# Performance work log

Measured on AMD Instinct MI355X. Metric: run time of the kernel, lower is better.

The kernel has to match this reference:

```python
import jax, jax.numpy as jnp
import numpy as np

B, D, S, H, L = 256, 7, 32, 512, 128  # batch, tree depth, n_symbols, hidden_size, latent_size
N = 2 ** D - 1  # nodes in complete binary tree, heap order (children of i are 2i+1, 2i+2)


def _xavier(key, shape):
    lim = float(np.sqrt(6.0 / (shape[0] + shape[1])))
    return jax.random.uniform(key, shape, jnp.float32, -lim, lim)


def setup_inputs():
    key = jax.random.key(0)
    ks = jax.random.split(key, 18)
    return {
        'symbols': jax.random.randint(ks[0], (B, N), 0, S, dtype=jnp.int32),
        'eps': jax.random.normal(ks[1], (B, L), jnp.float32),
        # Encoder GRU221: gate order [r, z, n], input weights act on one-hot symbol, hidden weights on cat(h_l, h_r)
        'ewi': _xavier(ks[2], (3 * H, S)),
        'ebi': jax.random.uniform(ks[3], (3 * H,), jnp.float32, -0.05, 0.05),
        'ewh': _xavier(ks[4], (3 * H, 2 * H)),
        'ebh': jax.random.uniform(ks[5], (3 * H,), jnp.float32, -0.05, 0.05),
        'h2mu_w': _xavier(ks[6], (L, H)),
        'h2mu_b': jax.random.uniform(ks[7], (L,), jnp.float32, -0.05, 0.05),
        'h2lv_w': _xavier(ks[8], (L, H)),
        'h2lv_b': jax.random.uniform(ks[9], (L,), jnp.float32, -0.05, 0.05),
        # Decoder
        'z2h_w': _xavier(ks[10], (H, L)),
        'z2h_b': jax.random.uniform(ks[11], (H,), jnp.float32, -0.05, 0.05),
        'h2o_w': _xavier(ks[12], (S, H)),
        'h2o_b': jax.random.uniform(ks[13], (S,), jnp.float32, -0.05, 0.05),
        # Decoder GRU122: gate order [r, z, n], each gate has 2H outputs (left/right child)
        'dwi': _xavier(ks[14], (6 * H, S)),
        'dbi': jax.random.uniform(ks[15], (6 * H,), jnp.float32, -0.05, 0.05),
        'dwh': _xavier(ks[16], (6 * H, H)),
        'dbh': jax.random.uniform(ks[17], (6 * H,), jnp.float32, -0.05, 0.05),
    }


def _hvae_forward(symbols, eps, ewi, ebi, ewh, ebh, h2mu_w, h2mu_b, h2lv_w, h2lv_b,
                  z2h_w, z2h_b, h2o_w, h2o_b, dwi, dbi, dwh, dbh):
    x_all = jax.nn.one_hot(symbols, S, dtype=jnp.float32)  # [B, N, S] node targets

    # ---- Encoder: GRU221 applied bottom-up, one batched step per tree level ----
    h = jnp.zeros((B, 2 ** D, H), jnp.float32)  # (absent) children of the deepest level
    for d in range(D - 1, -1, -1):
        n_d = 2 ** d
        x = x_all[:, n_d - 1: 2 * n_d - 1]       # [B, n_d, S] level-d symbols (heap order)
        hl, hr = h[:, 0::2], h[:, 1::2]           # [B, n_d, H] left/right child hiddens
        hcat = jnp.concatenate([hl, hr], axis=-1)
        gi = x @ ewi.T + ebi                       # [B, n_d, 3H]
        gh = hcat @ ewh.T + ebh
        r = jax.nn.sigmoid(gi[..., :H] + gh[..., :H])
        zg = jax.nn.sigmoid(gi[..., H:2 * H] + gh[..., H:2 * H])
        n = jnp.tanh(gi[..., 2 * H:] + r * gh[..., 2 * H:])
        h = (1.0 - zg) * n + zg * (hl + hr) * 0.5
    root = h[:, 0]                                 # [B, H]
    mu = root @ h2mu_w.T + h2mu_b                  # [B, L]
    logvar = root @ h2lv_w.T + h2lv_b
    zlat = mu + eps * jnp.exp(0.5 * logvar)        # reparameterized sample

    # ---- Decoder: GRU122 applied top-down, one batched step per tree level ----
    hidden = (zlat @ z2h_w.T + z2h_b)[:, None, :]  # [B, 1, H] root hidden
    preds = []
    for d in range(D):
        pred = hidden @ h2o_w.T + h2o_b            # [B, 2^d, S]
        preds.append(pred)
        if d < D - 1:
            a = jax.nn.softmax(pred, axis=-1)
            gi = a @ dwi.T + dbi                    # [B, 2^d, 6H]
            gh = hidden @ dwh.T + dbh
            r = jax.nn.sigmoid(gi[..., :2 * H] + gh[..., :2 * H])
            zg = jax.nn.sigmoid(gi[..., 2 * H:4 * H] + gh[..., 2 * H:4 * H])
            n = jnp.tanh(gi[..., 4 * H:] + r * gh[..., 4 * H:])
            dh = jnp.concatenate([hidden, hidden], axis=-1)  # h.repeat(1,1,2)
            out = (1.0 - zg) * n + zg * dh          # [B, 2^d, 2H]
            # torch.split -> (left, right); interleave as next level's hiddens (heap order)
            hidden = jnp.stack([out[..., :H], out[..., H:]], axis=2).reshape(B, 2 ** (d + 1), H)
    preds = jnp.concatenate(preds, axis=1)          # [B, N, S] per-node logits, level order
    return mu, logvar, preds


def reference(symbols, eps, ewi, ebi, ewh, ebh, h2mu_w, h2mu_b, h2lv_w, h2lv_b,
              z2h_w, z2h_b, h2o_w, h2o_b, dwi, dbi, dwh, dbh):
    return _hvae_forward(symbols, eps, ewi, ebi, ewh, ebh, h2mu_w, h2mu_b, h2lv_w, h2lv_b,
                         z2h_w, z2h_b, h2o_w, h2o_b, dwi, dbi, dwh, dbh)
```

## Files before the change

kernel.cpp:

```cpp
#include <hip/hip_runtime.h>
#include <hip/hip_bf16.h>

typedef unsigned short u16;
typedef unsigned int u32;
typedef __attribute__((ext_vector_type(8))) short short8;
typedef __attribute__((ext_vector_type(4))) float f32x4;

#define WAITV(N) asm volatile("s_waitcnt vmcnt(" #N ")" ::: "memory")

__device__ __forceinline__ float sigmoidf_(float x) { return 1.0f / (1.0f + expf(-x)); }
__device__ __forceinline__ float fsig(float x) {
    return __builtin_amdgcn_rcpf(1.0f + __expf(-x));
}
__device__ __forceinline__ float ftanh(float x) {
    x = fminf(fmaxf(x, -15.0f), 15.0f);
    float t = __expf(2.0f * x);
    return (t - 1.0f) * __builtin_amdgcn_rcpf(t + 1.0f);
}

__device__ __forceinline__ float bf2f(u16 u) {
    union { u32 i; float f; } v; v.i = ((u32)u) << 16; return v.f;
}
__device__ __forceinline__ u16 f2bf(float f) {
    union { float f; u32 i; } v; v.f = f;
    u32 lsb = (v.i >> 16) & 1u;
    v.i += 0x7fffu + lsb;
    return (u16)(v.i >> 16);
}

__device__ __forceinline__ void gload16(const u16* g, u16* l) {
    __builtin_amdgcn_global_load_lds(
        (const __attribute__((address_space(1))) u32*)g,
        (__attribute__((address_space(3))) u32*)l, 16, 0, 0);
}

__global__ __launch_bounds__(256) void prep(
    const float* __restrict__ ewh, const float* __restrict__ dwh,
    const float* __restrict__ dwi, const float* __restrict__ ewi,
    const float* __restrict__ h2o_w, const int* __restrict__ symbols,
    const float* __restrict__ ebi, const float* __restrict__ ebh,
    u16* __restrict__ ewh_b, u16* __restrict__ dwh_b, u16* __restrict__ dwi_b,
    u16* __restrict__ ewi_b, u16* __restrict__ wo_b, u16* __restrict__ oneh,
    u16* __restrict__ ltab)
{
    int idx = blockIdx.x * 256 + threadIdx.x;
    if (idx < 1572864) { ewh_b[idx] = f2bf(ewh[idx]); return; }
    idx -= 1572864;
    if (idx < 1572864) { dwh_b[idx] = f2bf(dwh[idx]); return; }
    idx -= 1572864;
    if (idx < 98304) { dwi_b[idx] = f2bf(dwi[idx]); return; }
    idx -= 98304;
    if (idx < 49152) { ewi_b[idx] = f2bf(ewi[idx]); return; }
    idx -= 49152;
    if (idx < 16384) { wo_b[idx] = f2bf(h2o_w[idx]); return; }
    idx -= 16384;
    if (idx < 1040384) {
        int col = idx & 31, row = idx >> 5;
        oneh[idx] = (col == symbols[row]) ? (u16)0x3F80 : (u16)0;
        return;
    }
    idx -= 1040384;
    if (idx < 16384) {
        int c = idx & 511, sym = idx >> 9;
        float r = sigmoidf_(ewi[c * 32 + sym]          + ebi[c]        + ebh[c]);
        float z = sigmoidf_(ewi[(512 + c) * 32 + sym]  + ebi[512 + c]  + ebh[512 + c]);
        float n = tanhf(    ewi[(1024 + c) * 32 + sym] + ebi[1024 + c] + r * ebh[1024 + c]);
        ltab[idx] = f2bf((1.0f - z) * n);
    }
}

template<int RF, bool LEAF>
__global__ __launch_bounds__(256, 2) void enc_tile(
    const u16* __restrict__ A, const u16* __restrict__ W,
    const u16* __restrict__ oneh, const u16* __restrict__ Wi,
    const u16* __restrict__ tab, const int* __restrict__ symbols,
    const float* __restrict__ ebi, const float* __restrict__ ebh,
    u16* __restrict__ hout, int dlog, int node_base)
{
    constexpr int BM = RF * 32;
    constexpr int NCA = BM / 64;
    constexpr int NS = 32;
    __shared__ alignas(16) u16 Als[2][BM * 32];
    __shared__ alignas(16) u16 Bls[2][192 * 32];
    const int tid  = threadIdx.x;
    const int lane = tid & 63;
    const int wid  = tid >> 6;
    const int wr = wid >> 1, wc = wid & 1;
    const int lr = lane & 15, lk = lane >> 4;
    const int m0 = blockIdx.x * BM;
    const int c0 = blockIdx.y * 64;
    const int mask = (1 << dlog) - 1;

    size_t a_goff[NCA]; int a_loff[NCA];
    int symL[NCA], symR[NCA];
#pragma unroll
    for (int j = 0; j < NCA; ++j) {
        int a = wid * NCA + j;
        int r_ = a * 16 + (lane >> 2);
        int kps = (lane & 3) ^ ((r_ >> 1) & 3);
        a_loff[j] = a * 512 + lane * 8;
        if constexpr (LEAF) {
            int rg = m0 + r_;
            int b_ = rg >> dlog, jj = rg & mask;
            int cbase = b_ * 127 + 2 * (node_base + jj) + 1;
            symL[j] = symbols[cbase];
            symR[j] = symbols[cbase + 1];
            a_goff[j] = kps * 8;
        } else {
            a_goff[j] = (size_t)(m0 + r_) * 1024 + kps * 8;
            symL[j] = symR[j] = 0;
        }
    }
    size_t b_goff[3]; int b_loff[3];
#pragma unroll
    for (int j = 0; j < 3; ++j) {
        int b = wid * 3 + j;
        int rr = b * 16 + (lane >> 2);
        int kps = (lane & 3) ^ ((rr >> 1) & 3);
        int grow = (rr >> 6) * 512 + c0 + (rr & 63);
        b_goff[j] = (size_t)grow * 1024 + kps * 8;
        b_loff[j] = b * 512 + lane * 8;
    }
    int a_roff[RF];
#pragma unroll
    for (int i = 0; i < RF; ++i) {
        int row = wr * (RF * 16) + i * 16 + lr;
        a_roff[i] = row * 32 + (lk ^ ((row >> 1) & 3)) * 8;
    }
    int b_roff[3][2];
#pragma unroll
    for (int s = 0; s < 3; ++s)
#pragma unroll
        for (int cf = 0; cf < 2; ++cf) {
            int row = s * 64 + wc * 32 + cf * 16 + lr;
            b_roff[s][cf] = row * 32 + (lk ^ ((row >> 1) & 3)) * 8;
        }

    f32x4 acc[4][2][RF];
#pragma unroll
    for (int s = 0; s < 4; ++s)
#pragma unroll
        for (int cf = 0; cf < 2; ++cf)
#pragma unroll
            for (int i = 0; i < RF; ++i) acc[s][cf][i] = (f32x4){0.f, 0.f, 0.f, 0.f};

    auto issue = [&](int stg) {
        const int buf = stg & 1;
        const int nk = stg * 32;
#pragma unroll
        for (int j = 0; j < NCA; ++j) {
            if constexpr (LEAF) {
                const u16* src = (nk < 512)
                    ? tab + (size_t)symL[j] * 512 + nk + a_goff[j]
                    : tab + (size_t)symR[j] * 512 + (nk - 512) + a_goff[j];
                gload16(src, &Als[buf][a_loff[j]]);
            } else {
                gload16(A + a_goff[j] + nk, &Als[buf][a_loff[j]]);
            }
        }
#pragma unroll
        for (int j = 0; j < 3; ++j) gload16(W + b_goff[j] + nk, &Bls[buf][b_loff[j]]);
    };
    auto compute = [&](int buf) {
        short8 a[RF];
#pragma unroll
        for (int i = 0; i < RF; ++i)
            a[i] = *reinterpret_cast<const short8*>(&Als[buf][a_roff[i]]);
#pragma unroll
        for (int s = 0; s < 3; ++s)
#pragma unroll
            for (int cf = 0; cf < 2; ++cf) {
                short8 b = *reinterpret_cast<const short8*>(&Bls[buf][b_roff[s][cf]]);
#pragma unroll
                for (int i = 0; i < RF; ++i)
                    acc[s][cf][i] = __builtin_amdgcn_mfma_f32_16x16x32_bf16(b, a[i], acc[s][cf][i], 0, 0, 0);
            }
    };

    issue(0);
    WAITV(0);
    __builtin_amdgcn_s_barrier();
    for (int t = 0; t < NS - 1; ++t) {
        issue(t + 1);
        compute(t & 1);
        WAITV(0);
        __builtin_amdgcn_s_barrier();
    }
    compute((NS - 1) & 1);

    {
        short8 oh[RF];
#pragma unroll
        for (int i = 0; i < RF; ++i) {
            int m = m0 + wr * (RF * 16) + i * 16 + lr;
            int b_ = m >> dlog, j_ = m & mask;
            oh[i] = *reinterpret_cast<const short8*>(
                oneh + (size_t)(b_ * 127 + node_base + j_) * 32 + lk * 8);
        }
#pragma unroll
        for (int s = 0; s < 3; ++s) {
            const int d = (s == 2) ? 3 : s;
#pragma unroll
            for (int cf = 0; cf < 2; ++cf) {
                short8 wb = *reinterpret_cast<const short8*>(
                    Wi + (size_t)(s * 512 + c0 + wc * 32 + cf * 16 + lr) * 32 + lk * 8);
#pragma unroll
                for (int i = 0; i < RF; ++i)
                    acc[d][cf][i] = __builtin_amdgcn_mfma_f32_16x16x32_bf16(wb, oh[i], acc[d][cf][i], 0, 0, 0);
            }
        }
    }

    float4 ebr4[2], ebz4[2], ebin4[2], ebhn4[2];
    int cb[2];
#pragma unroll
    for (int cf = 0; cf < 2; ++cf) {
        cb[cf] = c0 + wc * 32 + cf * 16 + lk * 4;
        float4 bi0 = *reinterpret_cast<const float4*>(ebi + cb[cf]);
        float4 bh0 = *reinterpret_cast<const float4*>(ebh + cb[cf]);
        float4 bi1 = *reinterpret_cast<const float4*>(ebi + 512 + cb[cf]);
        float4 bh1 = *reinterpret_cast<const float4*>(ebh + 512 + cb[cf]);
        ebr4[cf] = make_float4(bi0.x + bh0.x, bi0.y + bh0.y, bi0.z + bh0.z, bi0.w + bh0.w);
        ebz4[cf] = make_float4(bi1.x + bh1.x, bi1.y + bh1.y, bi1.z + bh1.z, bi1.w + bh1.w);
        ebin4[cf] = *reinterpret_cast<const float4*>(ebi + 1024 + cb[cf]);
        ebhn4[cf] = *reinterpret_cast<const float4*>(ebh + 1024 + cb[cf]);
    }
#pragma unroll
    for (int i = 0; i < RF; ++i) {
        int m = m0 + wr * (RF * 16) + i * 16 + lr;
        int symLm = 0, symRm = 0;
        if constexpr (LEAF) {
            int b_ = m >> dlog, jj = m & mask;
            int cbase_ = b_ * 127 + 2 * (node_base + jj) + 1;
            symLm = symbols[cbase_];
            symRm = symbols[cbase_ + 1];
        }
#pragma unroll
        for (int cf = 0; cf < 2; ++cf) {
            ushort4 hl4, hr4;
            if constexpr (LEAF) {
                hl4 = *reinterpret_cast<const ushort4*>(tab + (size_t)symLm * 512 + cb[cf]);
                hr4 = *reinterpret_cast<const ushort4*>(tab + (size_t)symRm * 512 + cb[cf]);
            } else {
                hl4 = *reinterpret_cast<const ushort4*>(A + (size_t)m * 1024 + cb[cf]);
                hr4 = *reinterpret_cast<const ushort4*>(A + (size_t)m * 1024 + 512 + cb[cf]);
            }
            const float eb_r[4] = {ebr4[cf].x, ebr4[cf].y, ebr4[cf].z, ebr4[cf].w};
            const float eb_z[4] = {ebz4[cf].x, ebz4[cf].y, ebz4[cf].z, ebz4[cf].w};
            const float eb_in[4] = {ebin4[cf].x, ebin4[cf].y, ebin4[cf].z, ebin4[cf].w};
            const float eb_hn[4] = {ebhn4[cf].x, ebhn4[cf].y, ebhn4[cf].z, ebhn4[cf].w};
            const u16 hlv[4] = {hl4.x, hl4.y, hl4.z, hl4.w};
            const u16 hrv[4] = {hr4.x, hr4.y, hr4.z, hr4.w};
            ushort4 outv;
            u16* ov = reinterpret_cast<u16*>(&outv);
#pragma unroll
            for (int r = 0; r < 4; ++r) {
                float rr_ = fsig(acc[0][cf][i][r] + eb_r[r]);
                float zz  = fsig(acc[1][cf][i][r] + eb_z[r]);
                float nn  = ftanh(acc[3][cf][i][r] + eb_in[r] + rr_ * (acc[2][cf][i][r] + eb_hn[r]));
                float hm = (bf2f(hlv[r]) + bf2f(hrv[r])) * 0.5f;
                ov[r] = f2bf((1.0f - zz) * nn + zz * hm);
            }
            *reinterpret_cast<ushort4*>(hout + (size_t)m * 512 + cb[cf]) = outv;
        }
    }
}

__global__ __launch_bounds__(256) void mid1(
    const u16* __restrict__ root, const float* __restrict__ h2mu_w,
    const float* __restrict__ h2mu_b, const float* __restrict__ h2lv_w,
    const float* __restrict__ h2lv_b, const float* __restrict__ eps,
    float* __restrict__ zlat, float* __restrict__ out_mu,
    float* __restrict__ out_lv)
{
    int b = blockIdx.x, t = threadIdx.x;
    __shared__ float rs[512];
    rs[t]       = bf2f(root[(size_t)b * 512 + t]);
    rs[t + 256] = bf2f(root[(size_t)b * 512 + t + 256]);
    __syncthreads();
    const float* w = (t < 128) ? (h2mu_w + (size_t)t * 512) : (h2lv_w + (size_t)(t - 128) * 512);
    float acc = 0.0f;
    for (int k = 0; k < 512; ++k) acc += rs[k] * w[k];
    acc += (t < 128) ? h2mu_b[t] : h2lv_b[t - 128];
    __shared__ float vals[256];
    vals[t] = acc;
    __syncthreads();
    if (t < 128) {
        float mu = vals[t], lv = vals[t + 128];
        float zl = mu + eps[b * 128 + t] * expf(0.5f * lv);
        zlat[b * 128 + t] = zl;
        out_mu[b * 128 + t] = mu;
        out_lv[b * 128 + t] = lv;
    }
}

__global__ __launch_bounds__(512) void mid2(
    const float* __restrict__ zlat, const float* __restrict__ z2h_w,
    const float* __restrict__ z2h_b, u16* __restrict__ hidden)
{
    int b = blockIdx.x, t = threadIdx.x;
    __shared__ float zs[128];
    if (t < 128) zs[t] = zlat[b * 128 + t];
    __syncthreads();
    float acc = z2h_b[t];
    for (int k = 0; k < 128; ++k) acc += zs[k] * z2h_w[(size_t)t * 128 + k];
    hidden[(size_t)b * 512 + t] = f2bf(acc);
}

__global__ __launch_bounds__(256) void pred_mfma(
    const u16* __restrict__ hidden, const u16* __restrict__ Wo,
    const float* __restrict__ h2o_b, u16* __restrict__ aout,
    float* __restrict__ preds_out, int dlog, int node_base, int write_a)
{
    const int lane = threadIdx.x & 63;
    const int wid  = threadIdx.x >> 6;
    const int lr = lane & 15, lk = lane >> 4;
    const int m0 = blockIdx.x * 64 + wid * 16;

    f32x4 acc0 = (f32x4){0.f, 0.f, 0.f, 0.f};
    f32x4 acc1 = (f32x4){0.f, 0.f, 0.f, 0.f};
    const u16* Arow = hidden + (size_t)(m0 + lr) * 512 + lk * 8;
    const u16* B0 = Wo + (size_t)lr * 512 + lk * 8;
    const u16* B1 = Wo + (size_t)(16 + lr) * 512 + lk * 8;
#pragma unroll
    for (int k0 = 0; k0 < 512; k0 += 32) {
        short8 a  = *reinterpret_cast<const short8*>(Arow + k0);
        short8 b0 = *reinterpret_cast<const short8*>(B0 + k0);
        short8 b1 = *reinterpret_cast<const short8*>(B1 + k0);
        acc0 = __builtin_amdgcn_mfma_f32_16x16x32_bf16(b0, a, acc0, 0, 0, 0);
        acc1 = __builtin_amdgcn_mfma_f32_16x16x32_bf16(b1, a, acc1, 0, 0, 0);
    }
    float4 bb0 = *reinterpret_cast<const float4*>(h2o_b + lk * 4);
    float4 bb1 = *reinterpret_cast<const float4*>(h2o_b + 16 + lk * 4);
    float p0[4], p1[4];
    p0[0] = acc0[0] + bb0.x; p0[1] = acc0[1] + bb0.y; p0[2] = acc0[2] + bb0.z; p0[3] = acc0[3] + bb0.w;
    p1[0] = acc1[0] + bb1.x; p1[1] = acc1[1] + bb1.y; p1[2] = acc1[2] + bb1.z; p1[3] = acc1[3] + bb1.w;
    float mx = fmaxf(fmaxf(fmaxf(p0[0], p0[1]), fmaxf(p0[2], p0[3])),
                     fmaxf(fmaxf(p1[0], p1[1]), fmaxf(p1[2], p1[3])));
    mx = fmaxf(mx, __shfl_xor(mx, 16));
    mx = fmaxf(mx, __shfl_xor(mx, 32));
    float e0[4], e1[4], s = 0.0f;
#pragma unroll
    for (int r = 0; r < 4; ++r) { e0[r] = __expf(p0[r] - mx); e1[r] = __expf(p1[r] - mx); s += e0[r] + e1[r]; }
    s += __shfl_xor(s, 16);
    s += __shfl_xor(s, 32);

    int m = m0 + lr;
    int b_ = m >> dlog, j_ = m & ((1 << dlog) - 1);
    size_t o = (size_t)(b_ * 127 + node_base + j_) * 32;
    *reinterpret_cast<float4*>(preds_out + o + lk * 4)      = make_float4(p0[0], p0[1], p0[2], p0[3]);
    *reinterpret_cast<float4*>(preds_out + o + 16 + lk * 4) = make_float4(p1[0], p1[1], p1[2], p1[3]);
    if (write_a) {
        float inv = __builtin_amdgcn_rcpf(s);
        ushort4 a0, a1;
        u16* av0 = reinterpret_cast<u16*>(&a0);
        u16* av1 = reinterpret_cast<u16*>(&a1);
#pragma unroll
        for (int r = 0; r < 4; ++r) { av0[r] = f2bf(e0[r] * inv); av1[r] = f2bf(e1[r] * inv); }
        *reinterpret_cast<ushort4*>(aout + (size_t)m * 32 + lk * 4)      = a0;
        *reinterpret_cast<ushort4*>(aout + (size_t)m * 32 + 16 + lk * 4) = a1;
    }
}

template<int RF>
__global__ __launch_bounds__(256, 2) void dec_tile(
    const u16* __restrict__ Hin, const u16* __restrict__ aB,
    const u16* __restrict__ Wh, const u16* __restrict__ Wi,
    const float* __restrict__ dbh, const float* __restrict__ dbi,
    u16* __restrict__ Hout)
{
    constexpr int BM = RF * 32;
    constexpr int NCA = BM / 64;
    constexpr int NS = 16;
    __shared__ alignas(16) u16 Als[2][BM * 32];
    __shared__ alignas(16) u16 Bls[2][192 * 32];
    const int tid  = threadIdx.x;
    const int lane = tid & 63;
    const int wid  = tid >> 6;
    const int wr = wid >> 1, wc = wid & 1;
    const int lr = lane & 15, lk = lane >> 4;
    const int m0 = blockIdx.x * BM;
    const int c0 = blockIdx.y * 64;

    size_t a_goff[NCA]; int a_loff[NCA];
#pragma unroll
    for (int j = 0; j < NCA; ++j) {
        int a = wid * NCA + j;
        int r_ = a * 16 + (lane >> 2);
        int kps = (lane & 3) ^ ((r_ >> 1) & 3);
        a_goff[j] = (size_t)(m0 + r_) * 512 + kps * 8;
        a_loff[j] = a * 512 + lane * 8;
    }
    size_t b_goff[3]; int b_loff[3];
#pragma unroll
    for (int j = 0; j < 3; ++j) {
        int b = wid * 3 + j;
        int rr = b * 16 + (lane >> 2);
        int kps = (lane & 3) ^ ((rr >> 1) & 3);
        int grow = (rr >> 6) * 1024 + c0 + (rr & 63);
        b_goff[j] = (size_t)grow * 512 + kps * 8;
        b_loff[j] = b * 512 + lane * 8;
    }
    int a_roff[RF];
#pragma unroll
    for (int i = 0; i < RF; ++i) {
        int row = wr * (RF * 16) + i * 16 + lr;
        a_roff[i] = row * 32 + (lk ^ ((row >> 1) & 3)) * 8;
    }
    int b_roff[3][2];
#pragma unroll
    for (int s = 0; s < 3; ++s)
#pragma unroll
        for (int cf = 0; cf < 2; ++cf) {
            int row = s * 64 + wc * 32 + cf * 16 + lr;
            b_roff[s][cf] = row * 32 + (lk ^ ((row >> 1) & 3)) * 8;
        }

    f32x4 acc[4][2][RF];
#pragma unroll
    for (int s = 0; s < 4; ++s)
#pragma unroll
        for (int cf = 0; cf < 2; ++cf)
#pragma unroll
            for (int i = 0; i < RF; ++i) acc[s][cf][i] = (f32x4){0.f, 0.f, 0.f, 0.f};

    auto issue = [&](int stg) {
        const int buf = stg & 1;
        const int nk = stg * 32;
#pragma unroll
        for (int j = 0; j < NCA; ++j) gload16(Hin + a_goff[j] + nk, &Als[buf][a_loff[j]]);
#pragma unroll
        for (int j = 0; j < 3; ++j) gload16(Wh + b_goff[j] + nk, &Bls[buf][b_loff[j]]);
    };
    auto compute = [&](int buf) {
        short8 a[RF];
#pragma unroll
        for (int i = 0; i < RF; ++i)
            a[i] = *reinterpret_cast<const short8*>(&Als[buf][a_roff[i]]);
#pragma unroll
        for (int s = 0; s < 3; ++s)
#pragma unroll
            for (int cf = 0; cf < 2; ++cf) {
                short8 b = *reinterpret_cast<const short8*>(&Bls[buf][b_roff[s][cf]]);
#pragma unroll
                for (int i = 0; i < RF; ++i)
                    acc[s][cf][i] = __builtin_amdgcn_mfma_f32_16x16x32_bf16(b, a[i], acc[s][cf][i], 0, 0, 0);
            }
    };

    issue(0);
    WAITV(0);
    __builtin_amdgcn_s_barrier();
    for (int t = 0; t < NS - 1; ++t) {
        issue(t + 1);
        compute(t & 1);
        WAITV(0);
        __builtin_amdgcn_s_barrier();
    }
    compute((NS - 1) & 1);

#pragma unroll
    for (int i = 0; i < RF; ++i) {
        short8 aw = *reinterpret_cast<const short8*>(
            aB + (size_t)(m0 + wr * (RF * 16) + i * 16 + lr) * 32 + lk * 8);
#pragma unroll
        for (int s = 0; s < 3; ++s) {
            const int d = (s == 2) ? 3 : s;
#pragma unroll
            for (int cf = 0; cf < 2; ++cf) {
                short8 b = *reinterpret_cast<const short8*>(
                    Wi + (size_t)(s * 1024 + c0 + wc * 32 + cf * 16 + lr) * 32 + lk * 8);
                acc[d][cf][i] = __builtin_amdgcn_mfma_f32_16x16x32_bf16(b, aw, acc[d][cf][i], 0, 0, 0);
            }
        }
    }

    float4 br4[2], bz4[2], bin4[2], bhn4[2];
    int cb[2];
#pragma unroll
    for (int cf = 0; cf < 2; ++cf) {
        cb[cf] = c0 + wc * 32 + cf * 16 + lk * 4;
        float4 h0 = *reinterpret_cast<const float4*>(dbh + cb[cf]);
        float4 i0 = *reinterpret_cast<const float4*>(dbi + cb[cf]);
        float4 h1 = *reinterpret_cast<const float4*>(dbh + 1024 + cb[cf]);
        float4 i1 = *reinterpret_cast<const float4*>(dbi + 1024 + cb[cf]);
        br4[cf] = make_float4(h0.x + i0.x, h0.y + i0.y, h0.z + i0.z, h0.w + i0.w);
        bz4[cf] = make_float4(h1.x + i1.x, h1.y + i1.y, h1.z + i1.z, h1.w + i1.w);
        bin4[cf] = *reinterpret_cast<const float4*>(dbi + 2048 + cb[cf]);
        bhn4[cf] = *reinterpret_cast<const float4*>(dbh + 2048 + cb[cf]);
    }
#pragma unroll
    for (int i = 0; i < RF; ++i) {
        int m = m0 + wr * (RF * 16) + i * 16 + lr;
#pragma unroll
        for (int cf = 0; cf < 2; ++cf) {
            ushort4 hid4 = *reinterpret_cast<const ushort4*>(Hin + (size_t)m * 512 + (cb[cf] & 511));
            const float b_r[4] = {br4[cf].x, br4[cf].y, br4[cf].z, br4[cf].w};
            const float b_z[4] = {bz4[cf].x, bz4[cf].y, bz4[cf].z, bz4[cf].w};
            const float b_in[4] = {bin4[cf].x, bin4[cf].y, bin4[cf].z, bin4[cf].w};
            const float b_hn[4] = {bhn4[cf].x, bhn4[cf].y, bhn4[cf].z, bhn4[cf].w};
            const u16 hv[4] = {hid4.x, hid4.y, hid4.z, hid4.w};
            ushort4 outv;
            u16* ov = reinterpret_cast<u16*>(&outv);
#pragma unroll
            for (int r = 0; r < 4; ++r) {
                float rr_ = fsig(acc[0][cf][i][r] + b_r[r]);
                float zz  = fsig(acc[1][cf][i][r] + b_z[r]);
                float nn  = ftanh(acc[3][cf][i][r] + b_in[r] + rr_ * (acc[2][cf][i][r] + b_hn[r]));
                ov[r] = f2bf((1.0f - zz) * nn + zz * bf2f(hv[r]));
            }
            *reinterpret_cast<ushort4*>(Hout + (size_t)m * 1024 + cb[cf]) = outv;
        }
    }
}

extern "C" void kernel_launch(void* const* d_in, const int* in_sizes, int n_in,
                              void* d_out, int out_size, void* d_ws, size_t ws_size,
                              hipStream_t stream) {
    const int*   symbols = (const int*)  d_in[0];
    const float* eps     = (const float*)d_in[1];
    const float* ewi     = (const float*)d_in[2];
    const float* ebi     = (const float*)d_in[3];
    const float* ewh     = (const float*)d_in[4];
    const float* ebh     = (const float*)d_in[5];
    const float* h2mu_w  = (const float*)d_in[6];
    const float* h2mu_b  = (const float*)d_in[7];
    const float* h2lv_w  = (const float*)d_in[8];
    const float* h2lv_b  = (const float*)d_in[9];
    const float* z2h_w   = (const float*)d_in[10];
    const float* z2h_b   = (const float*)d_in[11];
    const float* h2o_w   = (const float*)d_in[12];
    const float* h2o_b   = (const float*)d_in[13];
    const float* dwi     = (const float*)d_in[14];
    const float* dbi     = (const float*)d_in[15];
    const float* dwh     = (const float*)d_in[16];
    const float* dbh     = (const float*)d_in[17];

    float* out    = (float*)d_out;
    float* out_mu = out;
    float* out_lv = out + 256 * 128;
    float* out_pr = out + 2 * 256 * 128;

    u16* bufL  = (u16*)d_ws;
    u16* bufS  = bufL  + (size_t)16384 * 512;
    u16* ewh_b = bufS  + (size_t)8192 * 512;
    u16* dwh_b = ewh_b + (size_t)1536 * 1024;
    u16* dwi_b = dwh_b + (size_t)3072 * 512;
    u16* ewi_b = dwi_b + (size_t)3072 * 32;
    u16* wo_b  = ewi_b + (size_t)1536 * 32;
    u16* ltab  = wo_b  + (size_t)32 * 512;
    u16* oneh  = ltab  + (size_t)32 * 512;
    u16* aBuf  = oneh  + (size_t)32512 * 32;
    float* zlat = (float*)(aBuf + (size_t)8192 * 32);

    prep<<<(4366336 + 255) / 256, 256, 0, stream>>>(
        ewh, dwh, dwi, ewi, h2o_w, symbols, ebi, ebh,
        ewh_b, dwh_b, dwi_b, ewi_b, wo_b, oneh, ltab);

    enc_tile<4, true><<<dim3(64, 8), 256, 0, stream>>>(
        nullptr, ewh_b, oneh, ewi_b, ltab, symbols, ebi, ebh, bufS, 5, 31);
    const u16* src = bufS;
    u16*       dst = bufL;
    for (int d = 4; d >= 0; --d) {
        int M = 256 << d;
        if (M >= 4096)
            enc_tile<4, false><<<dim3(M / 128, 8), 256, 0, stream>>>(
                src, ewh_b, oneh, ewi_b, ltab, symbols, ebi, ebh, dst, d, (1 << d) - 1);
        else
            enc_tile<2, false><<<dim3(M / 64, 8), 256, 0, stream>>>(
                src, ewh_b, oneh, ewi_b, ltab, symbols, ebi, ebh, dst, d, (1 << d) - 1);
        const u16* t = src; src = dst; dst = (u16*)t;
    }
    mid1<<<256, 256, 0, stream>>>(src, h2mu_w, h2mu_b, h2lv_w, h2lv_b, eps, zlat, out_mu, out_lv);
    mid2<<<256, 512, 0, stream>>>(zlat, z2h_w, z2h_b, bufL);

    const u16* hsrc = bufL;
    u16*       hdst = bufS;
    for (int d = 0; d < 6; ++d) {
        int M = 256 << d;
        pred_mfma<<<M / 64, 256, 0, stream>>>(hsrc, wo_b, h2o_b, aBuf, out_pr, d, (1 << d) - 1, 1);
        if (M >= 4096)
            dec_tile<4><<<dim3(M / 128, 16), 256, 0, stream>>>(hsrc, aBuf, dwh_b, dwi_b, dbh, dbi, hdst);
        else
            dec_tile<2><<<dim3(M / 64, 16), 256, 0, stream>>>(hsrc, aBuf, dwh_b, dwi_b, dbh, dbi, hdst);
        const u16* t = hsrc; hsrc = hdst; hdst = (u16*)t;
    }
    pred_mfma<<<16384 / 64, 256, 0, stream>>>(hsrc, wo_b, h2o_b, aBuf, out_pr, 6, 63, 0);
}
```

Before: 348.7 us.

## Fuse output-logit GEMM and softmax into decoder tile kernel; merge mid kernels

The per-level prediction GEMM (hidden @ h2o_w) and its softmax now run inside dec_tile, reusing the A fragments already staged in LDS. The softmax probabilities go to shared memory instead of a global buffer. This removes one launch per decoder level and the global round trip of the probabilities. mid1 and mid2 are also merged into a single kernel. In exchange, every column block (16 along y) recomputes the same logits, which adds redundant MFMA work and Wo loads. It also adds accumulator registers in a kernel bounded at two blocks per SIMD.

```diff
diff --git a/kernel.cpp b/kernel.cpp
--- a/kernel.cpp
+++ b/kernel.cpp
@@ -266,15 +266,17 @@
     }
 }
 
-__global__ __launch_bounds__(256) void mid1(
+__global__ __launch_bounds__(256) void midf(
     const u16* __restrict__ root, const float* __restrict__ h2mu_w,
     const float* __restrict__ h2mu_b, const float* __restrict__ h2lv_w,
     const float* __restrict__ h2lv_b, const float* __restrict__ eps,
-    float* __restrict__ zlat, float* __restrict__ out_mu,
-    float* __restrict__ out_lv)
+    const float* __restrict__ z2h_w, const float* __restrict__ z2h_b,
+    float* __restrict__ out_mu, float* __restrict__ out_lv,
+    u16* __restrict__ hidden)
 {
     int b = blockIdx.x, t = threadIdx.x;
     __shared__ float rs[512];
+    __shared__ float zl[128];
     rs[t]       = bf2f(root[(size_t)b * 512 + t]);
     rs[t + 256] = bf2f(root[(size_t)b * 512 + t + 256]);
     __syncthreads();
@@ -287,30 +289,23 @@
     __syncthreads();
     if (t < 128) {
         float mu = vals[t], lv = vals[t + 128];
-        float zl = mu + eps[b * 128 + t] * expf(0.5f * lv);
-        zlat[b * 128 + t] = zl;
+        zl[t] = mu + eps[b * 128 + t] * expf(0.5f * lv);
         out_mu[b * 128 + t] = mu;
         out_lv[b * 128 + t] = lv;
     }
-}
-
-__global__ __launch_bounds__(512) void mid2(
-    const float* __restrict__ zlat, const float* __restrict__ z2h_w,
-    const float* __restrict__ z2h_b, u16* __restrict__ hidden)
-{
-    int b = blockIdx.x, t = threadIdx.x;
-    __shared__ float zs[128];
-    if (t < 128) zs[t] = zlat[b * 128 + t];
     __syncthreads();
-    float acc = z2h_b[t];
-    for (int k = 0; k < 128; ++k) acc += zs[k] * z2h_w[(size_t)t * 128 + k];
-    hidden[(size_t)b * 512 + t] = f2bf(acc);
+    for (int c = t; c < 512; c += 256) {
+        float a2 = z2h_b[c];
+        const float* wz = z2h_w + (size_t)c * 128;
+        for (int k = 0; k < 128; ++k) a2 += zl[k] * wz[k];
+        hidden[(size_t)b * 512 + c] = f2bf(a2);
+    }
 }
 
 __global__ __launch_bounds__(256) void pred_mfma(
     const u16* __restrict__ hidden, const u16* __restrict__ Wo,
-    const float* __restrict__ h2o_b, u16* __restrict__ aout,
-    float* __restrict__ preds_out, int dlog, int node_base, int write_a)
+    const float* __restrict__ h2o_b, float* __restrict__ preds_out,
+    int dlog, int node_base)
 {
     const int lane = threadIdx.x & 63;
     const int wid  = threadIdx.x >> 6;
@@ -335,39 +330,20 @@
     float p0[4], p1[4];
     p0[0] = acc0[0] + bb0.x; p0[1] = acc0[1] + bb0.y; p0[2] = acc0[2] + bb0.z; p0[3] = acc0[3] + bb0.w;
     p1[0] = acc1[0] + bb1.x; p1[1] = acc1[1] + bb1.y; p1[2] = acc1[2] + bb1.z; p1[3] = acc1[3] + bb1.w;
-    float mx = fmaxf(fmaxf(fmaxf(p0[0], p0[1]), fmaxf(p0[2], p0[3])),
-                     fmaxf(fmaxf(p1[0], p1[1]), fmaxf(p1[2], p1[3])));
-    mx = fmaxf(mx, __shfl_xor(mx, 16));
-    mx = fmaxf(mx, __shfl_xor(mx, 32));
-    float e0[4], e1[4], s = 0.0f;
-#pragma unroll
-    for (int r = 0; r < 4; ++r) { e0[r] = __expf(p0[r] - mx); e1[r] = __expf(p1[r] - mx); s += e0[r] + e1[r]; }
-    s += __shfl_xor(s, 16);
-    s += __shfl_xor(s, 32);
-
     int m = m0 + lr;
     int b_ = m >> dlog, j_ = m & ((1 << dlog) - 1);
     size_t o = (size_t)(b_ * 127 + node_base + j_) * 32;
     *reinterpret_cast<float4*>(preds_out + o + lk * 4)      = make_float4(p0[0], p0[1], p0[2], p0[3]);
     *reinterpret_cast<float4*>(preds_out + o + 16 + lk * 4) = make_float4(p1[0], p1[1], p1[2], p1[3]);
-    if (write_a) {
-        float inv = __builtin_amdgcn_rcpf(s);
-        ushort4 a0, a1;
-        u16* av0 = reinterpret_cast<u16*>(&a0);
-        u16* av1 = reinterpret_cast<u16*>(&a1);
-#pragma unroll
-        for (int r = 0; r < 4; ++r) { av0[r] = f2bf(e0[r] * inv); av1[r] = f2bf(e1[r] * inv); }
-        *reinterpret_cast<ushort4*>(aout + (size_t)m * 32 + lk * 4)      = a0;
-        *reinterpret_cast<ushort4*>(aout + (size_t)m * 32 + 16 + lk * 4) = a1;
-    }
 }
 
 template<int RF>
 __global__ __launch_bounds__(256, 2) void dec_tile(
-    const u16* __restrict__ Hin, const u16* __restrict__ aB,
-    const u16* __restrict__ Wh, const u16* __restrict__ Wi,
+    const u16* __restrict__ Hin, const u16* __restrict__ Wh,
+    const u16* __restrict__ Wi, const u16* __restrict__ Wo,
     const float* __restrict__ dbh, const float* __restrict__ dbi,
-    u16* __restrict__ Hout)
+    const float* __restrict__ h2o_b, u16* __restrict__ Hout,
+    float* __restrict__ preds_out, int dlog, int node_base)
 {
     constexpr int BM = RF * 32;
     constexpr int NCA = BM / 64;
@@ -381,6 +357,7 @@
     const int lr = lane & 15, lk = lane >> 4;
     const int m0 = blockIdx.x * BM;
     const int c0 = blockIdx.y * 64;
+    const int mask = (1 << dlog) - 1;
 
     size_t a_goff[NCA]; int a_loff[NCA];
 #pragma unroll
@@ -423,6 +400,11 @@
         for (int cf = 0; cf < 2; ++cf)
 #pragma unroll
             for (int i = 0; i < RF; ++i) acc[s][cf][i] = (f32x4){0.f, 0.f, 0.f, 0.f};
+    f32x4 accp[2][RF];
+#pragma unroll
+    for (int cf = 0; cf < 2; ++cf)
+#pragma unroll
+        for (int i = 0; i < RF; ++i) accp[cf][i] = (f32x4){0.f, 0.f, 0.f, 0.f};
 
     auto issue = [&](int stg) {
         const int buf = stg & 1;
@@ -432,7 +414,7 @@
 #pragma unroll
         for (int j = 0; j < 3; ++j) gload16(Wh + b_goff[j] + nk, &Bls[buf][b_loff[j]]);
     };
-    auto compute = [&](int buf) {
+    auto compute = [&](int buf, int t) {
         short8 a[RF];
 #pragma unroll
         for (int i = 0; i < RF; ++i)
@@ -446,6 +428,14 @@
                 for (int i = 0; i < RF; ++i)
                     acc[s][cf][i] = __builtin_amdgcn_mfma_f32_16x16x32_bf16(b, a[i], acc[s][cf][i], 0, 0, 0);
             }
+#pragma unroll
+        for (int cf = 0; cf < 2; ++cf) {
+            short8 wo = *reinterpret_cast<const short8*>(
+                Wo + (size_t)(cf * 16 + lr) * 512 + t * 32 + lk * 8);
+#pragma unroll
+            for (int i = 0; i < RF; ++i)
+                accp[cf][i] = __builtin_amdgcn_mfma_f32_16x16x32_bf16(wo, a[i], accp[cf][i], 0, 0, 0);
+        }
     };
 
     issue(0);
@@ -453,16 +443,61 @@
     __builtin_amdgcn_s_barrier();
     for (int t = 0; t < NS - 1; ++t) {
         issue(t + 1);
-        compute(t & 1);
+        compute(t & 1, t);
         WAITV(0);
         __builtin_amdgcn_s_barrier();
     }
-    compute((NS - 1) & 1);
+    compute((NS - 1) & 1, NS - 1);
+
+    u16* aLds = &Als[0][0];
+    {
+        float4 bb0 = *reinterpret_cast<const float4*>(h2o_b + lk * 4);
+        float4 bb1 = *reinterpret_cast<const float4*>(h2o_b + 16 + lk * 4);
+#pragma unroll
+        for (int i = 0; i < RF; ++i) {
+            float p0[4], p1[4];
+            p0[0] = accp[0][i][0] + bb0.x; p0[1] = accp[0][i][1] + bb0.y;
+            p0[2] = accp[0][i][2] + bb0.z; p0[3] = accp[0][i][3] + bb0.w;
+            p1[0] = accp[1][i][0] + bb1.x; p1[1] = accp[1][i][1] + bb1.y;
+            p1[2] = accp[1][i][2] + bb1.z; p1[3] = accp[1][i][3] + bb1.w;
+            float mx = fmaxf(fmaxf(fmaxf(p0[0], p0[1]), fmaxf(p0[2], p0[3])),
+                             fmaxf(fmaxf(p1[0], p1[1]), fmaxf(p1[2], p1[3])));
+            mx = fmaxf(mx, __shfl_xor(mx, 16));
+            mx = fmaxf(mx, __shfl_xor(mx, 32));
+            float e0[4], e1[4], s = 0.0f;
+#pragma unroll
+            for (int r = 0; r < 4; ++r) {
+                e0[r] = __expf(p0[r] - mx); e1[r] = __expf(p1[r] - mx);
+                s += e0[r] + e1[r];
+            }
+            s += __shfl_xor(s, 16);
+            s += __shfl_xor(s, 32);
+            int mloc = wr * (RF * 16) + i * 16 + lr;
+            int m = m0 + mloc;
+            if (blockIdx.y == 0 && wc == 0) {
+                int b_ = m >> dlog, j_ = m & mask;
+                size_t o = (size_t)(b_ * 127 + node_base + j_) * 32;
+                *reinterpret_cast<float4*>(preds_out + o + lk * 4)      = make_float4(p0[0], p0[1], p0[2], p0[3]);
+                *reinterpret_cast<float4*>(preds_out + o + 16 + lk * 4) = make_float4(p1[0], p1[1], p1[2], p1[3]);
+            }
+            if (wc == 0) {
+                float inv = __builtin_amdgcn_rcpf(s);
+                ushort4 a0, a1;
+                u16* av0 = reinterpret_cast<u16*>(&a0);
+                u16* av1 = reinterpret_cast<u16*>(&a1);
+#pragma unroll
+                for (int r = 0; r < 4; ++r) { av0[r] = f2bf(e0[r] * inv); av1[r] = f2bf(e1[r] * inv); }
+                *reinterpret_cast<ushort4*>(aLds + mloc * 32 + lk * 4)      = a0;
+                *reinterpret_cast<ushort4*>(aLds + mloc * 32 + 16 + lk * 4) = a1;
+            }
+        }
+    }
+    __builtin_amdgcn_s_barrier();
 
 #pragma unroll
     for (int i = 0; i < RF; ++i) {
-        short8 aw = *reinterpret_cast<const short8*>(
-            aB + (size_t)(m0 + wr * (RF * 16) + i * 16 + lr) * 32 + lk * 8);
+        int mloc = wr * (RF * 16) + i * 16 + lr;
+        short8 aw = *reinterpret_cast<const short8*>(aLds + mloc * 32 + lk * 8);
 #pragma unroll
         for (int s = 0; s < 3; ++s) {
             const int d = (s == 2) ? 3 : s;
@@ -550,8 +585,6 @@
     u16* wo_b  = ewi_b + (size_t)1536 * 32;
     u16* ltab  = wo_b  + (size_t)32 * 512;
     u16* oneh  = ltab  + (size_t)32 * 512;
-    u16* aBuf  = oneh  + (size_t)32512 * 32;
-    float* zlat = (float*)(aBuf + (size_t)8192 * 32);
 
     prep<<<(4366336 + 255) / 256, 256, 0, stream>>>(
         ewh, dwh, dwi, ewi, h2o_w, symbols, ebi, ebh,
@@ -571,19 +604,20 @@
                 src, ewh_b, oneh, ewi_b, ltab, symbols, ebi, ebh, dst, d, (1 << d) - 1);
         const u16* t = src; src = dst; dst = (u16*)t;
     }
-    mid1<<<256, 256, 0, stream>>>(src, h2mu_w, h2mu_b, h2lv_w, h2lv_b, eps, zlat, out_mu, out_lv);
-    mid2<<<256, 512, 0, stream>>>(zlat, z2h_w, z2h_b, bufL);
+    midf<<<256, 256, 0, stream>>>(src, h2mu_w, h2mu_b, h2lv_w, h2lv_b, eps,
+                                  z2h_w, z2h_b, out_mu, out_lv, bufL);
 
     const u16* hsrc = bufL;
     u16*       hdst = bufS;
     for (int d = 0; d < 6; ++d) {
         int M = 256 << d;
-        pred_mfma<<<M / 64, 256, 0, stream>>>(hsrc, wo_b, h2o_b, aBuf, out_pr, d, (1 << d) - 1, 1);
         if (M >= 4096)
-            dec_tile<4><<<dim3(M / 128, 16), 256, 0, stream>>>(hsrc, aBuf, dwh_b, dwi_b, dbh, dbi, hdst);
+            dec_tile<4><<<dim3(M / 128, 16), 256, 0, stream>>>(
+                hsrc, dwh_b, dwi_b, wo_b, dbh, dbi, h2o_b, hdst, out_pr, d, (1 << d) - 1);
         else
-            dec_tile<2><<<dim3(M / 64, 16), 256, 0, stream>>>(hsrc, aBuf, dwh_b, dwi_b, dbh, dbi, hdst);
+            dec_tile<2><<<dim3(M / 64, 16), 256, 0, stream>>>(
+                hsrc, dwh_b, dwi_b, wo_b, dbh, dbi, h2o_b, hdst, out_pr, d, (1 << d) - 1);
         const u16* t = hsrc; hsrc = hdst; hdst = (u16*)t;
     }
-    pred_mfma<<<16384 / 64, 256, 0, stream>>>(hsrc, wo_b, h2o_b, aBuf, out_pr, 6, 63, 0);
-}
+    pred_mfma<<<16384 / 64, 256, 0, stream>>>(hsrc, wo_b, h2o_b, out_pr, 6, 63);
+}
```

Result: no change. 347.8 us (-0.3%).
